# Optimization experiments

Hardware: AMD Instinct MI355X
Metric: run time of the kernel (lower is better)

The kernel has to match this reference:

```python
import jax, jax.numpy as jnp
import numpy as np

B, T, D = 8, 1, 4096
H_Q, H_KV, DH = 32, 8, 128
S = 8192
K_KEEP = 128
N_REP = H_Q // H_KV


def setup_inputs() -> dict:
    key = jax.random.key(0)
    ks = jax.random.split(key, 6)
    return {
        "hidden_states": jax.random.normal(ks[0], (B, T, D), jnp.float32),
        "attn_w": jax.random.uniform(ks[1], (B, H_Q, T, S), jnp.float32),
        "k": jax.random.normal(ks[2], (B, H_KV, S, DH), jnp.float32),
        "v": jax.random.normal(ks[3], (B, H_KV, S, DH), jnp.float32),
        "Wq": jax.random.normal(ks[4], (D, D), jnp.float32) * 0.02,
        "Wo": jax.random.normal(ks[5], (D, D), jnp.float32) * 0.02,
    }


def reference(hidden_states, attn_w, k, v, Wq, Wo):
    # importance of each cached token: mean attention over heads and queries
    importance = attn_w.mean(axis=(1, 2))                      # [B, S]
    _, topk_idx = jax.lax.top_k(importance, K_KEEP)            # [B, K]
    # gather pruned KV (per-batch token selection, shared across kv heads)
    gather = jax.vmap(lambda x, idx: x[:, idx, :])             # [H_kv,S,Dh],[K] -> [H_kv,K,Dh]
    k_new = gather(k, topk_idx)                                # [B, H_kv, K, Dh]
    v_new = gather(v, topk_idx)
    # recompute attention on the pruned set
    q = (hidden_states @ Wq.T).reshape(B, T, H_Q, DH).transpose(0, 2, 1, 3)  # [B,Hq,T,Dh]
    k_all = jnp.repeat(k_new, N_REP, axis=1)                   # repeat_kv -> [B,Hq,K,Dh]
    v_all = jnp.repeat(v_new, N_REP, axis=1)
    scores = jnp.einsum('bhtd,bhsd->bhts', q, k_all) / jnp.sqrt(jnp.float32(DH))
    probs = jax.nn.softmax(scores, axis=-1)                    # [B,Hq,T,K]
    ctx = jnp.einsum('bhts,bhsd->bhtd', probs, v_all)
    ctx = ctx.transpose(0, 2, 1, 3).reshape(B, T, H_Q * DH)
    out = ctx @ Wo.T                                           # [B,T,D]
    return out, probs
```

## Files before the change

### kernel.cpp

```cpp
#include <hip/hip_runtime.h>

#define S_TOK 8192
#define NB 8
#define HQ 32
#define HKV 8
#define DH 128
#define KK 128
#define DIM 4096
#define NCOL4 (DIM / 4)

__device__ __forceinline__ void gemv4(const float* __restrict__ W,
                                      const float* __restrict__ x,
                                      float* __restrict__ y,
                                      int r0, int t, float* red ) {
    const float4* wp0 = (const float4*)(W + (size_t)(r0 + 0) * DIM);
    const float4* wp1 = (const float4*)(W + (size_t)(r0 + 1) * DIM);
    const float4* wp2 = (const float4*)(W + (size_t)(r0 + 2) * DIM);
    const float4* wp3 = (const float4*)(W + (size_t)(r0 + 3) * DIM);
    const float4* x4 = (const float4*)x;
    float acc0[NB], acc1[NB], acc2[NB], acc3[NB];
#pragma unroll
    for (int b = 0; b < NB; ++b) { acc0[b] = 0.f; acc1[b] = 0.f; acc2[b] = 0.f; acc3[b] = 0.f; }
#pragma unroll
    for (int it = 0; it < 4; ++it) {
        const int c = t + it * 256;
        float4 w0 = wp0[c];
        float4 w1 = wp1[c];
        float4 w2 = wp2[c];
        float4 w3 = wp3[c];
#pragma unroll
        for (int b = 0; b < NB; ++b) {
            float4 xv = x4[(size_t)b * NCOL4 + c];
            acc0[b] += w0.x * xv.x + w0.y * xv.y + w0.z * xv.z + w0.w * xv.w;
            acc1[b] += w1.x * xv.x + w1.y * xv.y + w1.z * xv.z + w1.w * xv.w;
            acc2[b] += w2.x * xv.x + w2.y * xv.y + w2.z * xv.z + w2.w * xv.w;
            acc3[b] += w3.x * xv.x + w3.y * xv.y + w3.z * xv.z + w3.w * xv.w;
        }
    }
    const int lane = t & 63, wv = t >> 6;
#pragma unroll
    for (int b = 0; b < NB; ++b) {
#pragma unroll
        for (int o = 32; o > 0; o >>= 1) {
            acc0[b] += __shfl_down(acc0[b], o);
            acc1[b] += __shfl_down(acc1[b], o);
            acc2[b] += __shfl_down(acc2[b], o);
            acc3[b] += __shfl_down(acc3[b], o);
        }
    }
    if (lane == 0) {
#pragma unroll
        for (int b = 0; b < NB; ++b) {
            red[wv * 32 + 0 * 8 + b] = acc0[b];
            red[wv * 32 + 1 * 8 + b] = acc1[b];
            red[wv * 32 + 2 * 8 + b] = acc2[b];
            red[wv * 32 + 3 * 8 + b] = acc3[b];
        }
    }
    __syncthreads();
    if (t < 32) {
        float s = red[0 * 32 + t] + red[1 * 32 + t] + red[2 * 32 + t] + red[3 * 32 + t];
        int b = t & 7;
        int r = r0 + (t >> 3);
        y[(size_t)b * DIM + r] = s;
    }
}

__global__ __launch_bounds__(256) void imp_gemvq_kernel(const float* __restrict__ attn_w,
                                                        const float* __restrict__ Wq,
                                                        const float* __restrict__ hidden,
                                                        unsigned* __restrict__ impbits,
                                                        float* __restrict__ q) {
    __shared__ float redg[4 * 32];
    const int t = threadIdx.x;
    const int bl = blockIdx.x;

    if (bl < 256) {
        const int tok = bl * 256 + t;
        const int b = tok >> 13;
        const int s = tok & (S_TOK - 1);
        const float* p = attn_w + (size_t)b * HQ * S_TOK + s;
        float acc = 0.f;
#pragma unroll
        for (int h = 0; h < HQ; ++h) acc += p[(size_t)h * S_TOK];
        unsigned uu = __float_as_uint(acc * (1.0f / 32.0f));
        uu = (uu & 0x80000000u) ? ~uu : (uu | 0x80000000u);
        impbits[tok] = uu;
        return;
    }
    gemv4(Wq, hidden, q, (bl - 256) * 4, t, redg);
}

__global__ __launch_bounds__(512) void attn_topk_kernel(const unsigned* __restrict__ impbits,
                                                        const float* __restrict__ q,
                                                        const float* __restrict__ k,
                                                        const float* __restrict__ v,
                                                        float* __restrict__ ctx,
                                                        float* __restrict__ probs_out) {
    __shared__ __align__(16) unsigned mb[S_TOK];
    __shared__ __align__(16) int hist[256];
    __shared__ unsigned sprefix;
    __shared__ int skrem;
    __shared__ int nsel;
    __shared__ unsigned selb[KK];
    __shared__ int seli[KK];
    __shared__ float qs[DH];
    __shared__ float scs[KK];
    __shared__ float ps[KK];
    __shared__ float red2[2];
    __shared__ float red3[2];
    __shared__ float part[3][DH];

    const int t = threadIdx.x;
    const int bl = blockIdx.x;
    const int b = bl >> 5, h = bl & 31, kvh = h >> 2;

    if (t < DH) qs[t] = q[(size_t)(b * HQ + h) * DH + t] * 0.088388347648318447f;

    const unsigned* ip = impbits + (size_t)b * S_TOK;
    for (int i = t; i < S_TOK; i += 512) mb[i] = ip[i];
    if (t == 0) { sprefix = 0u; skrem = KK; nsel = 0; }
    __syncthreads();

    for (int shift = 24; shift >= 0; shift -= 8) {
        if (t < 256) hist[t] = 0;
        __syncthreads();
        const unsigned pfx = sprefix;
        const int krem = skrem;
        if (shift == 24) {
            for (int i = t; i < S_TOK; i += 512) {
                int bin = mb[i] >> 24;
                unsigned long long rem = __ballot(1);
                while (rem) {
                    int fl = (int)__builtin_ctzll(rem);
                    int fbin = __shfl(bin, fl);
                    unsigned long long match = __ballot(bin == fbin);
                    if ((t & 63) == fl) atomicAdd(&hist[fbin], (int)__popcll(match));
                    rem &= ~match;
                }
            }
        } else {
            const unsigned pmask = 0xFFFFFFFFu << (shift + 8);
            for (int i = t; i < S_TOK; i += 512) {
                unsigned u = mb[i];
                if ((u & pmask) == pfx) atomicAdd(&hist[(u >> shift) & 255], 1);
            }
        }
        __syncthreads();
        if (t < 64) {
            int4 h4 = *(const int4*)&hist[252 - 4 * t];
            int h0 = h4.w, h1 = h4.z, h2 = h4.y, h3 = h4.x;
            int c0 = h0, c1 = c0 + h1, c2 = c1 + h2, c3 = c2 + h3;
            int inc = c3;
#pragma unroll
            for (int o = 1; o < 64; o <<= 1) {
                int yv = __shfl_up(inc, o);
                if (t >= o) inc += yv;
            }
            int excl = inc - c3;
            int cand = -1, before = 0;
            if      (excl + c0 >= krem) { cand = 0; before = excl; }
            else if (excl + c1 >= krem) { cand = 1; before = excl + c0; }
            else if (excl + c2 >= krem) { cand = 2; before = excl + c1; }
            else if (excl + c3 >= krem) { cand = 3; before = excl + c2; }
            unsigned long long ball = __ballot(cand >= 0);
            int win = (int)__builtin_ctzll(ball);
            if (t == win) {
                int p = 4 * t + cand;
                sprefix = pfx | ((unsigned)(255 - p) << shift);
                skrem = krem - before;
            }
        }
        __syncthreads();
    }
    const unsigned T = sprefix;

    for (int i = t; i < S_TOK; i += 512) {
        unsigned u = mb[i];
        if (u > T) {
            int p = atomicAdd(&nsel, 1);
            selb[p] = u; seli[p] = i;
        }
    }
    __syncthreads();
    const int g = nsel;
    const int r = KK - g;

    if (t < 64) {
        int found = 0;
        for (int base0 = 0; base0 < S_TOK && found < r; base0 += 64) {
            bool is_tie = (mb[base0 + t] == T);
            unsigned long long ball = __ballot(is_tie);
            int pos = (int)__popcll(ball & ((1ull << t) - 1ull));
            if (is_tie && found + pos < r) {
                selb[g + found + pos] = T;
                seli[g + found + pos] = base0 + t;
            }
            found += (int)__popcll(ball);
        }
    }
    __syncthreads();

    for (int ksz = 2; ksz <= KK; ksz <<= 1) {
        for (int j = ksz >> 1; j > 0; j >>= 1) {
            if (t < KK) {
                int i = t, l = i ^ j;
                if (l > i) {
                    bool up = ((i & ksz) == 0);
                    unsigned ab = selb[i], cb = selb[l];
                    int ai = seli[i], ci = seli[l];
                    bool aFirst = (ab > cb) || (ab == cb && ai < ci);
                    if (up ? !aFirst : aFirst) {
                        selb[i] = cb; selb[l] = ab;
                        seli[i] = ci; seli[l] = ai;
                    }
                }
            }
            __syncthreads();
        }
    }

    {
        const int tok = t >> 2, qpart = t & 3;
        const float4* k4 = (const float4*)(k +
            ((size_t)(b * HKV + kvh) * S_TOK + seli[tok]) * DH + qpart * 32);
        float sc = 0.f;
#pragma unroll
        for (int d4 = 0; d4 < 8; ++d4) {
            float4 kv = k4[d4];
            int d0 = qpart * 32 + d4 * 4;
            sc += qs[d0] * kv.x + qs[d0 + 1] * kv.y + qs[d0 + 2] * kv.z + qs[d0 + 3] * kv.w;
        }
        sc += __shfl_xor(sc, 1);
        sc += __shfl_xor(sc, 2);
        if (qpart == 0) scs[tok] = sc;
    }
    __syncthreads();

    float sc = (t < KK) ? scs[t] : -3.4e38f;
    if (t < KK) {
        float m = sc;
        for (int o = 32; o > 0; o >>= 1) m = fmaxf(m, __shfl_down(m, o));
        if ((t & 63) == 0) red2[t >> 6] = m;
    }
    __syncthreads();
    const float mx = fmaxf(red2[0], red2[1]);
    float p = 0.f;
    if (t < KK) {
        p = expf(sc - mx);
        float sm = p;
        for (int o = 32; o > 0; o >>= 1) sm += __shfl_down(sm, o);
        if ((t & 63) == 0) red3[t >> 6] = sm;
    }
    __syncthreads();
    if (t < KK) {
        p /= (red3[0] + red3[1]);
        ps[t] = p;
        probs_out[(size_t)(b * HQ + h) * KK + t] = p;
    }
    __syncthreads();

    {
        const int d = t & (DH - 1), grp = t >> 7;
        const float* vbase = v + (size_t)(b * HKV + kvh) * S_TOK * DH;
        float acc = 0.f;
        const int s0 = grp * 32;
#pragma unroll 4
        for (int s2 = s0; s2 < s0 + 32; ++s2) {
            acc += ps[s2] * vbase[(size_t)seli[s2] * DH + d];
        }
        if (grp) part[grp - 1][d] = acc;
        __syncthreads();
        if (grp == 0)
            ctx[(size_t)(b * HQ + h) * DH + d] = acc + part[0][d] + part[1][d] + part[2][d];
    }
}

__global__ __launch_bounds__(256) void gemv_wo_kernel(const float* __restrict__ Wo,
                                                      const float* __restrict__ ctx,
                                                      float* __restrict__ out) {
    __shared__ float redg[4 * 32];
    gemv4(Wo, ctx, out, blockIdx.x * 4, threadIdx.x, redg);
}

extern "C" void kernel_launch(void* const* d_in, const int* in_sizes, int n_in,
                              void* d_out, int out_size, void* d_ws, size_t ws_size,
                              hipStream_t stream) {
    const float* hidden = (const float*)d_in[0];
    const float* attn_w = (const float*)d_in[1];
    const float* k      = (const float*)d_in[2];
    const float* v      = (const float*)d_in[3];
    const float* Wq     = (const float*)d_in[4];
    const float* Wo     = (const float*)d_in[5];

    float* out   = (float*)d_out;
    float* probs = out + NB * DIM;

    char* ws = (char*)d_ws;
    unsigned* impbits = (unsigned*)ws;
    float* q     = (float*)(ws + 262144);
    float* ctx   = (float*)(ws + 393216);

    imp_gemvq_kernel<<<256 + DIM / 4, 256, 0, stream>>>(attn_w, Wq, hidden, impbits, q);
    attn_topk_kernel<<<NB * HQ, 512, 0, stream>>>(impbits, q, k, v, ctx, probs);
    gemv_wo_kernel<<<DIM / 4, 256, 0, stream>>>(Wo, ctx, out);
}
```

Before: 72.51 us.

## Fuse Wo projection into attention kernel via per-head atomic accumulation

Drops the separate Wo GEMV launch. Each attention block now multiplies its 128-wide head context slice against the matching Wo columns and atomically adds partial results into the output. The first kernel gains 8 extra blocks that zero the output buffer beforehand. This saves a kernel launch and the ctx round trip, at the cost of 32x more atomics per output element and Wo being read once per batch (8x) instead of once overall.

```diff
diff --git a/kernel.cpp b/kernel.cpp
--- a/kernel.cpp
+++ b/kernel.cpp
@@ -70,7 +70,8 @@
                                                         const float* __restrict__ Wq,
                                                         const float* __restrict__ hidden,
                                                         unsigned* __restrict__ impbits,
-                                                        float* __restrict__ q) {
+                                                        float* __restrict__ q,
+                                                        float* __restrict__ out) {
     __shared__ float redg[4 * 32];
     const int t = threadIdx.x;
     const int bl = blockIdx.x;
@@ -88,15 +89,24 @@
         impbits[tok] = uu;
         return;
     }
-    gemv4(Wq, hidden, q, (bl - 256) * 4, t, redg);
+    if (bl < 264) {
+        float4 z = {0.f, 0.f, 0.f, 0.f};
+        float4* o4 = (float4*)out;
+        const int base = (bl - 256) * 1024 + t;
+#pragma unroll
+        for (int i = 0; i < 4; ++i) o4[base + i * 256] = z;
+        return;
+    }
+    gemv4(Wq, hidden, q, (bl - 264) * 4, t, redg);
 }
 
-__global__ __launch_bounds__(512) void attn_topk_kernel(const unsigned* __restrict__ impbits,
-                                                        const float* __restrict__ q,
-                                                        const float* __restrict__ k,
-                                                        const float* __restrict__ v,
-                                                        float* __restrict__ ctx,
-                                                        float* __restrict__ probs_out) {
+__global__ __launch_bounds__(512) void attn_topk_wo_kernel(const unsigned* __restrict__ impbits,
+                                                           const float* __restrict__ q,
+                                                           const float* __restrict__ k,
+                                                           const float* __restrict__ v,
+                                                           const float* __restrict__ Wo,
+                                                           float* __restrict__ out,
+                                                           float* __restrict__ probs_out) {
     __shared__ __align__(16) unsigned mb[S_TOK];
     __shared__ __align__(16) int hist[256];
     __shared__ unsigned sprefix;
@@ -110,6 +120,7 @@
     __shared__ float red2[2];
     __shared__ float red3[2];
     __shared__ float part[3][DH];
+    __shared__ __align__(16) float ctxs[DH];
 
     const int t = threadIdx.x;
     const int bl = blockIdx.x;
@@ -272,15 +283,35 @@
         if (grp) part[grp - 1][d] = acc;
         __syncthreads();
         if (grp == 0)
-            ctx[(size_t)(b * HQ + h) * DH + d] = acc + part[0][d] + part[1][d] + part[2][d];
-    }
-}
-
-__global__ __launch_bounds__(256) void gemv_wo_kernel(const float* __restrict__ Wo,
-                                                      const float* __restrict__ ctx,
-                                                      float* __restrict__ out) {
-    __shared__ float redg[4 * 32];
-    gemv4(Wo, ctx, out, blockIdx.x * 4, threadIdx.x, redg);
+            ctxs[d] = acc + part[0][d] + part[1][d] + part[2][d];
+    }
+    __syncthreads();
+
+    {
+        const int team = t >> 2, j = t & 3;
+        const float4* cx = (const float4*)ctxs;
+        float4 c0 = cx[j * 8 + 0], c1 = cx[j * 8 + 1], c2 = cx[j * 8 + 2], c3 = cx[j * 8 + 3];
+        float4 c4 = cx[j * 8 + 4], c5 = cx[j * 8 + 5], c6 = cx[j * 8 + 6], c7 = cx[j * 8 + 7];
+        float* ob = out + (size_t)b * DIM;
+#pragma unroll 4
+        for (int i = 0; i < 32; ++i) {
+            const int rr = team + (i << 7);
+            const float4* w4 = (const float4*)(Wo + (size_t)rr * DIM + h * DH + j * 32);
+            float4 w0 = w4[0], w1 = w4[1], w2 = w4[2], w3 = w4[3];
+            float4 w5 = w4[4], w6 = w4[5], w7 = w4[6], w8 = w4[7];
+            float dot = w0.x * c0.x + w0.y * c0.y + w0.z * c0.z + w0.w * c0.w
+                      + w1.x * c1.x + w1.y * c1.y + w1.z * c1.z + w1.w * c1.w
+                      + w2.x * c2.x + w2.y * c2.y + w2.z * c2.z + w2.w * c2.w
+                      + w3.x * c3.x + w3.y * c3.y + w3.z * c3.z + w3.w * c3.w
+                      + w5.x * c4.x + w5.y * c4.y + w5.z * c4.z + w5.w * c4.w
+                      + w6.x * c5.x + w6.y * c5.y + w6.z * c5.z + w6.w * c5.w
+                      + w7.x * c6.x + w7.y * c6.y + w7.z * c6.z + w7.w * c6.w
+                      + w8.x * c7.x + w8.y * c7.y + w8.z * c7.z + w8.w * c7.w;
+            dot += __shfl_xor(dot, 1);
+            dot += __shfl_xor(dot, 2);
+            if (j == 0) atomicAdd(&ob[rr], dot);
+        }
+    }
 }
 
 extern "C" void kernel_launch(void* const* d_in, const int* in_sizes, int n_in,
@@ -299,9 +330,8 @@
     char* ws = (char*)d_ws;
     unsigned* impbits = (unsigned*)ws;
     float* q     = (float*)(ws + 262144);
-    float* ctx   = (float*)(ws + 393216);
-
-    imp_gemvq_kernel<<<256 + DIM / 4, 256, 0, stream>>>(attn_w, Wq, hidden, impbits, q);
-    attn_topk_kernel<<<NB * HQ, 512, 0, stream>>>(impbits, q, k, v, ctx, probs);
-    gemv_wo_kernel<<<DIM / 4, 256, 0, stream>>>(Wo, ctx, out);
+
+    imp_gemvq_kernel<<<256 + 8 + DIM / 4, 256, 0, stream>>>(attn_w, Wq, hidden,
+                                                            impbits, q, out);
+    attn_topk_wo_kernel<<<NB * HQ, 512, 0, stream>>>(impbits, q, k, v, Wo, out, probs);
 }
```

Result: slower. 122.8 us (+69.3%).
